# Performance work log

Hardware: AMD Instinct MI355X
Metric: run time of the kernel (lower is better)

Reference implementation:

```python
import jax, jax.numpy as jnp
import numpy as np

N, E = 100000, 1600000
D_IN, D_H, D_OUT = 128, 128, 64


def setup_inputs() -> dict:
    key = jax.random.key(0)
    ks = jax.random.split(key, 5)
    x = jax.random.normal(ks[0], (N, D_IN), dtype=jnp.float32)
    edge_index = jax.random.randint(ks[1], (2, E), 0, N, dtype=jnp.int64)
    edge_weight = jax.random.uniform(ks[2], (E,), dtype=jnp.float32)
    W1 = jax.random.normal(ks[3], (D_IN, D_H), dtype=jnp.float32) / np.sqrt(D_IN).astype(np.float32)
    b1 = jnp.zeros((D_H,), jnp.float32)
    W2 = jax.random.normal(ks[4], (D_H, D_OUT), dtype=jnp.float32) / np.sqrt(D_H).astype(np.float32)
    b2 = jnp.zeros((D_OUT,), jnp.float32)
    return {"x": x, "edge_index": edge_index, "edge_weight": edge_weight,
            "W1": W1, "b1": b1, "W2": W2, "b2": b2}


def gcn_conv(x, row, col, ew, W, b):
    # PyG GCNConv: symmetric gcn_norm with self-loops (fill value 1.0)
    n = x.shape[0]
    deg = jax.ops.segment_sum(ew, col, num_segments=n) + 1.0  # +1 from self-loop
    dis = jax.lax.rsqrt(deg)                                   # deg^{-1/2}
    norm = dis[row] * ew * dis[col]                            # [E]
    xw = x @ W                                                 # [N, out]
    agg = jax.ops.segment_sum(norm[:, None] * xw[row], col, num_segments=n)
    agg = agg + (dis * dis)[:, None] * xw                      # self-loop messages (weight 1)
    return agg + b


def reference(x, edge_index, edge_weight, W1, b1, W2, b2):
    row, col = edge_index[0], edge_index[1]
    h = jax.nn.relu(gcn_conv(x, row, col, edge_weight, W1, b1))
    # F.dropout(training=False) is identity in eval mode
    return gcn_conv(h, row, col, edge_weight, W2, b2)
```

## Files before the change

### kernel.cpp

```cpp
#include <hip/hip_runtime.h>
#include <stdint.h>

typedef unsigned int uint32;
typedef _Float16 f16x8 __attribute__((ext_vector_type(8)));
typedef float f32x4 __attribute__((ext_vector_type(4)));


#define NPBSH 6
#define NPB 64
#define PBLK 256
#define CAP 2048

__global__ void detect_kernel(const int* __restrict__ ei, int* flag) {
    if (threadIdx.x == 0 && blockIdx.x == 0) {
        int z = 0;
        for (int i = 0; i < 16; ++i) z |= ei[2 * i + 1];
        *flag = (z == 0) ? 1 : 0;
    }
}

__device__ inline int chunk_map(int blk) {
    return (blk & 7) * (PBLK / 8) + (blk >> 3);
}

__global__ __launch_bounds__(512) void p1_hist(const void* __restrict__ ei, int E, int NB,
                                               int chunk, const int* __restrict__ flag,
                                               int* __restrict__ cnt_bb) {
    extern __shared__ int h[];
    const int t = threadIdx.x;
    const int blk = chunk_map(blockIdx.x);
    for (int i = t; i < NB; i += 512) h[i] = 0;
    __syncthreads();
    const int is64 = *flag;
    const int* e32 = (const int*)ei;
    const long long* e64 = (const long long*)ei;
    const int e0 = blk * chunk;
    const int e1 = min(e0 + chunk, E);
    for (int e = e0 + t; e < e1; e += 512) {
        int c = is64 ? (int)e64[(size_t)E + e] : e32[(size_t)E + e];
        atomicAdd(&h[c >> NPBSH], 1);
    }
    __syncthreads();
    for (int i = t; i < NB; i += 512) cnt_bb[(size_t)blk * NB + i] = h[i];
}

__global__ __launch_bounds__(PBLK) void s1_colscan(const int* __restrict__ cnt_bb,
                                                   int* __restrict__ boff_rel,
                                                   int* __restrict__ tb, int NB) {
    __shared__ int sm[PBLK];
    const int t = threadIdx.x, b = blockIdx.x;
    int v = cnt_bb[(size_t)t * NB + b];
    sm[t] = v;
    __syncthreads();
    for (int off = 1; off < PBLK; off <<= 1) {
        int u = (t >= off) ? sm[t - off] : 0;
        __syncthreads();
        sm[t] += u;
        __syncthreads();
    }
    boff_rel[(size_t)t * NB + b] = sm[t] - v;
    if (t == PBLK - 1) tb[b] = sm[PBLK - 1];
}

__global__ __launch_bounds__(1024) void scan_kernel(const int* __restrict__ cnt,
                                                    int* __restrict__ ptr, int n) {
    __shared__ int sm[1024];
    const int t = threadIdx.x;
    const int chunk = (n + 1023) / 1024;
    const int start = t * chunk;
    const int end = min(start + chunk, n);
    int s = 0;
    for (int i = start; i < end; ++i) s += cnt[i];
    sm[t] = s;
    __syncthreads();
    for (int off = 1; off < 1024; off <<= 1) {
        int v = (t >= off) ? sm[t - off] : 0;
        __syncthreads();
        sm[t] += v;
        __syncthreads();
    }
    int run = (t == 0) ? 0 : sm[t - 1];
    for (int i = start; i < end; ++i) { ptr[i] = run; run += cnt[i]; }
    if (start < n && end == n) ptr[n] = run;
}

__global__ __launch_bounds__(512) void p2_scatter(const void* __restrict__ ei,
                                                  const float* __restrict__ ew,
                                                  int E, int NB, int chunk,
                                                  const int* __restrict__ flag,
                                                  const int* __restrict__ bstart,
                                                  const int* __restrict__ boff_rel,
                                                  int2* __restrict__ bktrec) {
    extern __shared__ int cur[];
    const int t = threadIdx.x;
    const int blk = chunk_map(blockIdx.x);
    for (int i = t; i < NB; i += 512)
        cur[i] = bstart[i] + boff_rel[(size_t)blk * NB + i];
    __syncthreads();
    const int is64 = *flag;
    const int* e32 = (const int*)ei;
    const long long* e64 = (const long long*)ei;
    const int e0 = blk * chunk;
    const int e1 = min(e0 + chunk, E);
    for (int e = e0 + t; e < e1; e += 512) {
        int r, c;
        if (is64) { r = (int)e64[e]; c = (int)e64[(size_t)E + e]; }
        else      { r = e32[e];      c = e32[(size_t)E + e]; }
        int b = c >> NPBSH;
        int pos = atomicAdd(&cur[b], 1);
        bktrec[pos] = make_int2(r | ((c & (NPB - 1)) << 20), __float_as_int(ew[e]));
    }
}

__global__ __launch_bounds__(256) void p3_build(const int* __restrict__ bstart,
                                                const int2* __restrict__ bktrec,
                                                int* __restrict__ ptr, int* __restrict__ rows_s,
                                                float* __restrict__ ws_s, float* __restrict__ dis,
                                                int n, int NB, int E) {
    __shared__ int inp[CAP];
    __shared__ float inw[CAP];
    __shared__ int outr[CAP];
    __shared__ float outw[CAP];
    __shared__ int h[NPB], ex[NPB + 1], cu[NPB];
    const int t = threadIdx.x, b = blockIdx.x;
    const int base = bstart[b];
    const int eb = bstart[b + 1] - base;
    const int j0 = b << NPBSH;
    const int ncount = min(NPB, n - j0);
    if (t < NPB) { h[t] = 0; cu[t] = 0; }
    __syncthreads();

    if (eb <= CAP) {
        for (int i = t; i < eb; i += 256) {
            int2 rc = bktrec[base + i];
            inp[i] = rc.x;
            inw[i] = __int_as_float(rc.y);
            atomicAdd(&h[(rc.x >> 20) & 63], 1);
        }
        __syncthreads();
        if (t == 0) {
            int run = 0;
            for (int j = 0; j < NPB; ++j) { ex[j] = run; run += h[j]; }
            ex[NPB] = run;
        }
        __syncthreads();
        for (int i = t; i < eb; i += 256) {
            int v = inp[i];
            int cl = (v >> 20) & 63;
            int d = ex[cl] + atomicAdd(&cu[cl], 1);
            outr[d] = v & 0xFFFFF;
            outw[d] = inw[i];
        }
        __syncthreads();
        for (int i = t; i < eb; i += 256) {
            rows_s[base + i] = outr[i];
            ws_s[base + i] = outw[i];
        }
        if (t < ncount) {
            ptr[j0 + t] = base + ex[t];
            float s = 0.f;
            for (int i = ex[t]; i < ex[t] + h[t]; ++i) s += outw[i];
            dis[j0 + t] = rsqrtf(s + 1.0f);
        }
    } else {
        for (int i = t; i < eb; i += 256) atomicAdd(&h[(bktrec[base + i].x >> 20) & 63], 1);
        __syncthreads();
        if (t == 0) {
            int run = 0;
            for (int j = 0; j < NPB; ++j) { ex[j] = run; run += h[j]; }
            ex[NPB] = run;
        }
        __syncthreads();
        for (int i = t; i < eb; i += 256) {
            int2 rc = bktrec[base + i];
            int cl = (rc.x >> 20) & 63;
            int d = ex[cl] + atomicAdd(&cu[cl], 1);
            rows_s[base + d] = rc.x & 0xFFFFF;
            ws_s[base + d] = __int_as_float(rc.y);
        }
        __syncthreads();
        if (t < ncount) {
            ptr[j0 + t] = base + ex[t];
            float s = 0.f;
            for (int i = base + ex[t]; i < base + ex[t] + h[t]; ++i) s += ws_s[i];
            dis[j0 + t] = rsqrtf(s + 1.0f);
        }
    }
    if (b == NB - 1 && t == 0) ptr[n] = E;
    if (b == NB - 1 && t < 8) {
        rows_s[E + t] = 0;
        ws_s[E + t] = 0.f;
    }
}

__global__ void fold_kernel(const int* __restrict__ rows_s, float* __restrict__ ws_s,
                            const float* __restrict__ dis, int E) {
    for (int e = blockIdx.x * blockDim.x + threadIdx.x; e < E;
         e += gridDim.x * blockDim.x)
        ws_s[e] *= dis[rows_s[e]];
}

__device__ inline uint32 pack2h(float a, float b) {
    unsigned short ua = __builtin_bit_cast(unsigned short, (_Float16)a);
    unsigned short ub = __builtin_bit_cast(unsigned short, (_Float16)b);
    return (uint32)ua | ((uint32)ub << 16);
}
__device__ inline float h2lo(uint32 g) {
    return (float)__builtin_bit_cast(_Float16, (unsigned short)(g & 0xFFFFu));
}
__device__ inline float h2hi(uint32 g) {
    return (float)__builtin_bit_cast(_Float16, (unsigned short)(g >> 16));
}

__device__ inline int kposb(int k) {
    return ((k >> 5) << 6) + (((k >> 2) & 3) << 4) + (((k >> 4) & 1) << 3) + ((k & 3) << 1);
}

template <int DOUT, bool PACKED>
__global__ __launch_bounds__(256, 2) void mgemm_kernel(const void* __restrict__ Xv,
                                                       const float* __restrict__ W,
                                                       unsigned short* __restrict__ Y,
                                                       int n) {
    constexpr int NC = DOUT / 16;
    __shared__ __align__(16) unsigned short Xl[128 * 128];
    __shared__ __align__(16) unsigned short Wl[DOUT * 128];
    const int t = threadIdx.x;
    const int row0 = blockIdx.x * 128;

    for (int i = t * 4; i < 128 * 128; i += 1024) {
        int r = i >> 7, k = i & 127;
        uint2 st;
        if (PACKED) {
            uint2 v = {0u, 0u};
            if (row0 + r < n)
                v = *(const uint2*)((const uint32*)Xv + (size_t)(row0 + r) * 64 + (k >> 1));
            st = v;
        } else {
            float4 v = {0.f, 0.f, 0.f, 0.f};
            if (row0 + r < n)
                v = *(const float4*)((const float*)Xv + (size_t)(row0 + r) * 128 + k);
            st.x = pack2h(v.x, v.y);
            st.y = pack2h(v.z, v.w);
        }
        *(uint2*)((char*)Xl + r * 256 + (kposb(k) ^ ((r & 7) << 4))) = st;
    }
    for (int i = t; i < 128 * (DOUT / 4); i += 256) {
        int k = i / (DOUT / 4);
        int c0 = (i % (DOUT / 4)) * 4;
        float4 wv = *(const float4*)(W + (size_t)k * DOUT + c0);
        float a[4] = {wv.x, wv.y, wv.z, wv.w};
        int kb = kposb(k);
#pragma unroll
        for (int j = 0; j < 4; ++j) {
            int c = c0 + j;
            *(unsigned short*)((char*)Wl + c * 256 + (kb ^ ((c & 7) << 4))) =
                __builtin_bit_cast(unsigned short, (_Float16)a[j]);
        }
    }
    __syncthreads();

    const int l = t & 63;
    const int w = t >> 6;
    const int lr = l & 15;
    const int lq = l >> 4;
    const int rbase = w * 32;
    const int swz = (lr & 7) << 4;

    f32x4 acc[2][NC];
#pragma unroll
    for (int i = 0; i < 2; ++i)
#pragma unroll
        for (int c = 0; c < NC; ++c) acc[i][c] = (f32x4){0.f, 0.f, 0.f, 0.f};

#pragma unroll
    for (int ks = 0; ks < 4; ++ks) {
        const int fo = ks * 64 + lq * 16;
        f16x8 a0 = *(const f16x8*)((const char*)Xl + (rbase + lr) * 256 + (fo ^ swz));
        f16x8 a1 = *(const f16x8*)((const char*)Xl + (rbase + 16 + lr) * 256 + (fo ^ swz));
#pragma unroll
        for (int c = 0; c < NC; ++c) {
            f16x8 b = *(const f16x8*)((const char*)Wl + (c * 16 + lr) * 256 + (fo ^ swz));
            acc[0][c] = __builtin_amdgcn_mfma_f32_16x16x32_f16(a0, b, acc[0][c], 0, 0, 0);
            acc[1][c] = __builtin_amdgcn_mfma_f32_16x16x32_f16(a1, b, acc[1][c], 0, 0, 0);
        }
    }

#pragma unroll
    for (int i = 0; i < 2; ++i) {
#pragma unroll
        for (int c = 0; c < NC; ++c) {
#pragma unroll
            for (int reg = 0; reg < 4; ++reg) {
                int row = row0 + rbase + i * 16 + lq * 4 + reg;
                if (row < n)
                    Y[(size_t)row * DOUT + c * 16 + lr] =
                        __builtin_bit_cast(unsigned short, (_Float16)acc[i][c][reg]);
            }
        }
    }
}

__global__ __launch_bounds__(256) void prop128_kernel(const uint32* __restrict__ xwb,
                                                      const float* __restrict__ dis,
                                                      const int* __restrict__ ptr,
                                                      const int* __restrict__ rows_s,
                                                      const float* __restrict__ ws_s,
                                                      const float* __restrict__ bias,
                                                      uint32* __restrict__ out, int n) {
    const int wid = threadIdx.x >> 6;
    const int lane = threadIdx.x & 63;
    const int half = lane >> 5;
    const int dlane = lane & 31;
    const int v = blockIdx.x * 4 + wid;
    if (v >= n) return;

    const int beg = __builtin_amdgcn_readfirstlane(ptr[v]);
    const int end = __builtin_amdgcn_readfirstlane(ptr[v + 1]);
    const float dv = dis[v];

    float a0 = 0.f, a1 = 0.f, a2 = 0.f, a3 = 0.f;
#pragma unroll 4
    for (int g = beg & ~1; g < end; g += 2) {
        int2 r2 = *(const int2*)(rows_s + g);
        float2 w2 = *(const float2*)(ws_s + g);
        int e = g + half;
        int r = half ? r2.y : r2.x;
        float w = half ? w2.y : w2.x;
        w = (e >= beg && e < end) ? w : 0.f;
        uint2 q = *(const uint2*)(xwb + (size_t)r * 64 + dlane * 2);
        a0 += w * h2lo(q.x);
        a1 += w * h2hi(q.x);
        a2 += w * h2lo(q.y);
        a3 += w * h2hi(q.y);
    }
    a0 += __shfl_xor(a0, 32);
    a1 += __shfl_xor(a1, 32);
    a2 += __shfl_xor(a2, 32);
    a3 += __shfl_xor(a3, 32);

    if (half == 0) {
        uint2 q = *(const uint2*)(xwb + (size_t)v * 64 + dlane * 2);
        float4 bi = *(const float4*)(bias + dlane * 4);
        float r0 = dv * a0 + dv * dv * h2lo(q.x) + bi.x;
        float r1 = dv * a1 + dv * dv * h2hi(q.x) + bi.y;
        float r2 = dv * a2 + dv * dv * h2lo(q.y) + bi.z;
        float r3 = dv * a3 + dv * dv * h2hi(q.y) + bi.w;
        r0 = fmaxf(r0, 0.f);
        r1 = fmaxf(r1, 0.f);
        r2 = fmaxf(r2, 0.f);
        r3 = fmaxf(r3, 0.f);
        uint2 o = {pack2h(r0, r1), pack2h(r2, r3)};
        *(uint2*)(out + (size_t)v * 64 + dlane * 2) = o;
    }
}

__global__ __launch_bounds__(256) void prop64_kernel(const uint32* __restrict__ xwb,
                                                     const float* __restrict__ dis,
                                                     const int* __restrict__ ptr,
                                                     const int* __restrict__ rows_s,
                                                     const float* __restrict__ ws_s,
                                                     const float* __restrict__ bias,
                                                     float* __restrict__ out, int n) {
    const int wid = threadIdx.x >> 6;
    const int lane = threadIdx.x & 63;
    const int q4 = lane >> 4;
    const int dlane = lane & 15;
    const int v = blockIdx.x * 4 + wid;
    if (v >= n) return;

    const int beg = __builtin_amdgcn_readfirstlane(ptr[v]);
    const int end = __builtin_amdgcn_readfirstlane(ptr[v + 1]);
    const float dv = dis[v];

    float a0 = 0.f, a1 = 0.f, a2 = 0.f, a3 = 0.f;
#pragma unroll 4
    for (int g = beg & ~3; g < end; g += 4) {
        int4 r4 = *(const int4*)(rows_s + g);
        float4 w4 = *(const float4*)(ws_s + g);
        int e = g + q4;
        int r = (q4 & 2) ? ((q4 & 1) ? r4.w : r4.z) : ((q4 & 1) ? r4.y : r4.x);
        float w = (q4 & 2) ? ((q4 & 1) ? w4.w : w4.z) : ((q4 & 1) ? w4.y : w4.x);
        w = (e >= beg && e < end) ? w : 0.f;
        uint2 q = *(const uint2*)(xwb + (size_t)r * 32 + dlane * 2);
        a0 += w * h2lo(q.x);
        a1 += w * h2hi(q.x);
        a2 += w * h2lo(q.y);
        a3 += w * h2hi(q.y);
    }
    a0 += __shfl_xor(a0, 16);
    a1 += __shfl_xor(a1, 16);
    a2 += __shfl_xor(a2, 16);
    a3 += __shfl_xor(a3, 16);
    a0 += __shfl_xor(a0, 32);
    a1 += __shfl_xor(a1, 32);
    a2 += __shfl_xor(a2, 32);
    a3 += __shfl_xor(a3, 32);

    if (lane < 16) {
        uint2 q = *(const uint2*)(xwb + (size_t)v * 32 + dlane * 2);
        float4 bi = *(const float4*)(bias + dlane * 4);
        float4 o;
        o.x = dv * a0 + dv * dv * h2lo(q.x) + bi.x;
        o.y = dv * a1 + dv * dv * h2hi(q.x) + bi.y;
        o.z = dv * a2 + dv * dv * h2lo(q.y) + bi.z;
        o.w = dv * a3 + dv * dv * h2hi(q.y) + bi.w;
        *(float4*)(out + (size_t)v * 64 + dlane * 4) = o;
    }
}

extern "C" void kernel_launch(void* const* d_in, const int* in_sizes, int n_in,
                              void* d_out, int out_size, void* d_ws, size_t ws_size,
                              hipStream_t stream) {
    const float* x  = (const float*)d_in[0];
    const void*  ei = d_in[1];
    const float* ew = (const float*)d_in[2];
    const float* W1 = (const float*)d_in[3];
    const float* b1 = (const float*)d_in[4];
    const float* W2 = (const float*)d_in[5];
    const float* b2 = (const float*)d_in[6];
    float* out = (float*)d_out;

    const int n = in_sizes[0] / 128;
    const int E = in_sizes[2];
    const int NB = (n + NPB - 1) >> NPBSH;
    const int chunk = (E + PBLK - 1) / PBLK;

    char* p = (char*)d_ws;
    size_t o = 0;
    auto alloc = [&](size_t bytes) -> void* {
        void* q = p + o;
        o += (bytes + 255) & ~(size_t)255;
        return q;
    };
    int*    flag     = (int*)alloc(4);
    int*    cnt_bb   = (int*)alloc((size_t)PBLK * NB * 4);
    int*    boff_rel = (int*)alloc((size_t)PBLK * NB * 4);
    int*    tb       = (int*)alloc((size_t)NB * 4);
    int*    bstart   = (int*)alloc(((size_t)NB + 1) * 4);
    int*    ptr      = (int*)alloc(((size_t)n + 1) * 4);
    float*  dis      = (float*)alloc((size_t)n * 4);
    int2*   bktrec   = (int2*)alloc((size_t)E * 8);
    int*    rows_s   = (int*)alloc(((size_t)E + 8) * 4);
    float*  ws_s     = (float*)alloc(((size_t)E + 8) * 4);
    uint32* bufA     = (uint32*)alloc((size_t)n * 64 * 4);
    uint32* bufB     = (uint32*)alloc((size_t)n * 64 * 4);

    const int gblk = (n + 127) / 128;

    detect_kernel<<<1, 64, 0, stream>>>((const int*)ei, flag);
    p1_hist<<<PBLK, 512, NB * 4, stream>>>(ei, E, NB, chunk, flag, cnt_bb);
    s1_colscan<<<NB, PBLK, 0, stream>>>(cnt_bb, boff_rel, tb, NB);
    scan_kernel<<<1, 1024, 0, stream>>>(tb, bstart, NB);
    p2_scatter<<<PBLK, 512, NB * 4, stream>>>(ei, ew, E, NB, chunk, flag, bstart,
                                              boff_rel, bktrec);
    p3_build<<<NB, 256, 0, stream>>>(bstart, bktrec, ptr, rows_s, ws_s, dis, n, NB, E);
    fold_kernel<<<2048, 256, 0, stream>>>(rows_s, ws_s, dis, E);

    mgemm_kernel<128, false><<<gblk, 256, 0, stream>>>(x, W1, (unsigned short*)bufA, n);
    prop128_kernel<<<(n + 3) / 4, 256, 0, stream>>>(bufA, dis, ptr, rows_s, ws_s, b1, bufB, n);
    mgemm_kernel<64, true><<<gblk, 256, 0, stream>>>(bufB, W2, (unsigned short*)bufA, n);
    prop64_kernel<<<(n + 3) / 4, 256, 0, stream>>>(bufA, dis, ptr, rows_s, ws_s, b2, out, n);
}
```

Measured before the change: 229.7 us.

## Store GEMM outputs in column-sliced layout and propagate per slice for cache locality

```diff
diff --git a/kernel.cpp b/kernel.cpp
--- a/kernel.cpp
+++ b/kernel.cpp
@@ -10,6 +10,7 @@
 #define NPB 64
 #define PBLK 256
 #define CAP 2048
+#define PCH 1024
 
 __global__ void detect_kernel(const int* __restrict__ ei, int* flag) {
     if (threadIdx.x == 0 && blockIdx.x == 0) {
@@ -233,7 +234,8 @@
         if (PACKED) {
             uint2 v = {0u, 0u};
             if (row0 + r < n)
-                v = *(const uint2*)((const uint32*)Xv + (size_t)(row0 + r) * 64 + (k >> 1));
+                v = *(const uint2*)((const uint32*)Xv +
+                                    ((size_t)(k >> 4) * n + (row0 + r)) * 8 + ((k & 15) >> 1));
             st = v;
         } else {
             float4 v = {0.f, 0.f, 0.f, 0.f};
@@ -293,118 +295,67 @@
             for (int reg = 0; reg < 4; ++reg) {
                 int row = row0 + rbase + i * 16 + lq * 4 + reg;
                 if (row < n)
-                    Y[(size_t)row * DOUT + c * 16 + lr] =
+                    Y[((size_t)c * n + row) * 16 + lr] =
                         __builtin_bit_cast(unsigned short, (_Float16)acc[i][c][reg]);
             }
         }
     }
 }
 
-__global__ __launch_bounds__(256) void prop128_kernel(const uint32* __restrict__ xwb,
-                                                      const float* __restrict__ dis,
-                                                      const int* __restrict__ ptr,
-                                                      const int* __restrict__ rows_s,
-                                                      const float* __restrict__ ws_s,
-                                                      const float* __restrict__ bias,
-                                                      uint32* __restrict__ out, int n) {
+template <int SLICES, int LS, bool RELU, bool F32OUT>
+__global__ __launch_bounds__(256) void props_kernel(const uint32* __restrict__ table,
+                                                    const float* __restrict__ dis,
+                                                    const int* __restrict__ ptr,
+                                                    const int* __restrict__ rows_s,
+                                                    const float* __restrict__ ws_s,
+                                                    const float* __restrict__ bias,
+                                                    void* __restrict__ out, int n) {
+    const int s = blockIdx.x & (SLICES - 1);
+    const int chunk = blockIdx.x >> LS;
     const int wid = threadIdx.x >> 6;
     const int lane = threadIdx.x & 63;
-    const int half = lane >> 5;
-    const int dlane = lane & 31;
-    const int v = blockIdx.x * 4 + wid;
-    if (v >= n) return;
-
-    const int beg = __builtin_amdgcn_readfirstlane(ptr[v]);
-    const int end = __builtin_amdgcn_readfirstlane(ptr[v + 1]);
-    const float dv = dis[v];
-
-    float a0 = 0.f, a1 = 0.f, a2 = 0.f, a3 = 0.f;
-#pragma unroll 4
-    for (int g = beg & ~1; g < end; g += 2) {
-        int2 r2 = *(const int2*)(rows_s + g);
-        float2 w2 = *(const float2*)(ws_s + g);
-        int e = g + half;
-        int r = half ? r2.y : r2.x;
-        float w = half ? w2.y : w2.x;
-        w = (e >= beg && e < end) ? w : 0.f;
-        uint2 q = *(const uint2*)(xwb + (size_t)r * 64 + dlane * 2);
-        a0 += w * h2lo(q.x);
-        a1 += w * h2hi(q.x);
-        a2 += w * h2lo(q.y);
-        a3 += w * h2hi(q.y);
-    }
-    a0 += __shfl_xor(a0, 32);
-    a1 += __shfl_xor(a1, 32);
-    a2 += __shfl_xor(a2, 32);
-    a3 += __shfl_xor(a3, 32);
-
-    if (half == 0) {
-        uint2 q = *(const uint2*)(xwb + (size_t)v * 64 + dlane * 2);
-        float4 bi = *(const float4*)(bias + dlane * 4);
-        float r0 = dv * a0 + dv * dv * h2lo(q.x) + bi.x;
-        float r1 = dv * a1 + dv * dv * h2hi(q.x) + bi.y;
-        float r2 = dv * a2 + dv * dv * h2lo(q.y) + bi.z;
-        float r3 = dv * a3 + dv * dv * h2hi(q.y) + bi.w;
-        r0 = fmaxf(r0, 0.f);
-        r1 = fmaxf(r1, 0.f);
-        r2 = fmaxf(r2, 0.f);
-        r3 = fmaxf(r3, 0.f);
-        uint2 o = {pack2h(r0, r1), pack2h(r2, r3)};
-        *(uint2*)(out + (size_t)v * 64 + dlane * 2) = o;
-    }
-}
-
-__global__ __launch_bounds__(256) void prop64_kernel(const uint32* __restrict__ xwb,
-                                                     const float* __restrict__ dis,
-                                                     const int* __restrict__ ptr,
-                                                     const int* __restrict__ rows_s,
-                                                     const float* __restrict__ ws_s,
-                                                     const float* __restrict__ bias,
-                                                     float* __restrict__ out, int n) {
-    const int wid = threadIdx.x >> 6;
-    const int lane = threadIdx.x & 63;
-    const int q4 = lane >> 4;
-    const int dlane = lane & 15;
-    const int v = blockIdx.x * 4 + wid;
-    if (v >= n) return;
-
-    const int beg = __builtin_amdgcn_readfirstlane(ptr[v]);
-    const int end = __builtin_amdgcn_readfirstlane(ptr[v + 1]);
-    const float dv = dis[v];
-
-    float a0 = 0.f, a1 = 0.f, a2 = 0.f, a3 = 0.f;
-#pragma unroll 4
-    for (int g = beg & ~3; g < end; g += 4) {
-        int4 r4 = *(const int4*)(rows_s + g);
-        float4 w4 = *(const float4*)(ws_s + g);
-        int e = g + q4;
-        int r = (q4 & 2) ? ((q4 & 1) ? r4.w : r4.z) : ((q4 & 1) ? r4.y : r4.x);
-        float w = (q4 & 2) ? ((q4 & 1) ? w4.w : w4.z) : ((q4 & 1) ? w4.y : w4.x);
-        w = (e >= beg && e < end) ? w : 0.f;
-        uint2 q = *(const uint2*)(xwb + (size_t)r * 32 + dlane * 2);
-        a0 += w * h2lo(q.x);
-        a1 += w * h2hi(q.x);
-        a2 += w * h2lo(q.y);
-        a3 += w * h2hi(q.y);
-    }
-    a0 += __shfl_xor(a0, 16);
-    a1 += __shfl_xor(a1, 16);
-    a2 += __shfl_xor(a2, 16);
-    a3 += __shfl_xor(a3, 16);
-    a0 += __shfl_xor(a0, 32);
-    a1 += __shfl_xor(a1, 32);
-    a2 += __shfl_xor(a2, 32);
-    a3 += __shfl_xor(a3, 32);
-
-    if (lane < 16) {
-        uint2 q = *(const uint2*)(xwb + (size_t)v * 32 + dlane * 2);
-        float4 bi = *(const float4*)(bias + dlane * 4);
-        float4 o;
-        o.x = dv * a0 + dv * dv * h2lo(q.x) + bi.x;
-        o.y = dv * a1 + dv * dv * h2hi(q.x) + bi.y;
-        o.z = dv * a2 + dv * dv * h2lo(q.y) + bi.z;
-        o.w = dv * a3 + dv * dv * h2hi(q.y) + bi.w;
-        *(float4*)(out + (size_t)v * 64 + dlane * 4) = o;
+    const int eslot = lane >> 3;
+    const int d = lane & 7;
+    const int gw = chunk * 4 + wid;
+    const int stride = PCH * 4;
+
+    const uint32* slice = table + (size_t)s * n * 8;
+    const float2 bi = *(const float2*)(bias + s * 16 + d * 2);
+
+    for (int v = gw; v < n; v += stride) {
+        const int beg = __builtin_amdgcn_readfirstlane(ptr[v]);
+        const int end = __builtin_amdgcn_readfirstlane(ptr[v + 1]);
+        const float dv = dis[v];
+
+        float a0 = 0.f, a1 = 0.f;
+        for (int g = beg; g < end; g += 8) {
+            int e = g + eslot;
+            float w = ws_s[e];
+            int r = rows_s[e];
+            if (e >= end) w = 0.f;
+            uint32 val = slice[(size_t)r * 8 + d];
+            a0 += w * h2lo(val);
+            a1 += w * h2hi(val);
+        }
+        a0 += __shfl_xor(a0, 8);
+        a1 += __shfl_xor(a1, 8);
+        a0 += __shfl_xor(a0, 16);
+        a1 += __shfl_xor(a1, 16);
+        a0 += __shfl_xor(a0, 32);
+        a1 += __shfl_xor(a1, 32);
+
+        if (eslot == 0) {
+            uint32 self = slice[(size_t)v * 8 + d];
+            float r0 = dv * a0 + dv * dv * h2lo(self) + bi.x;
+            float r1 = dv * a1 + dv * dv * h2hi(self) + bi.y;
+            if (RELU) { r0 = fmaxf(r0, 0.f); r1 = fmaxf(r1, 0.f); }
+            if (F32OUT) {
+                float2 o = {r0, r1};
+                *(float2*)((float*)out + (size_t)v * (SLICES * 16) + s * 16 + d * 2) = o;
+            } else {
+                ((uint32*)out)[((size_t)s * n + v) * 8 + d] = pack2h(r0, r1);
+            }
+        }
     }
 }
 
@@ -457,7 +408,9 @@
     fold_kernel<<<2048, 256, 0, stream>>>(rows_s, ws_s, dis, E);
 
     mgemm_kernel<128, false><<<gblk, 256, 0, stream>>>(x, W1, (unsigned short*)bufA, n);
-    prop128_kernel<<<(n + 3) / 4, 256, 0, stream>>>(bufA, dis, ptr, rows_s, ws_s, b1, bufB, n);
+    props_kernel<8, 3, true, false><<<8 * PCH, 256, 0, stream>>>(bufA, dis, ptr, rows_s,
+                                                                 ws_s, b1, bufB, n);
     mgemm_kernel<64, true><<<gblk, 256, 0, stream>>>(bufB, W2, (unsigned short*)bufA, n);
-    prop64_kernel<<<(n + 3) / 4, 256, 0, stream>>>(bufA, dis, ptr, rows_s, ws_s, b2, out, n);
-}
+    props_kernel<4, 2, false, true><<<4 * PCH, 256, 0, stream>>>(bufA, dis, ptr, rows_s,
+                                                                 ws_s, b2, out, n);
+}
```

Result: slower. 464.5 us (+102.2%).
